# Performance work log

Hardware: AMD Instinct MI355X
Metric: run time of the kernel (lower is better)

The kernel has to match this reference:

```python
import jax, jax.numpy as jnp
from jax import lax
import numpy as np

WIN = (9, 9, 9)
NUM_CH = 5       # Ii, Ji, I2, J2, IJ stacked on channel dim, grouped conv


def setup_inputs() -> dict:
    key = jax.random.key(0)
    k1, k2 = jax.random.split(key)
    shape = (1, 1, 128, 160, 192)
    y_true = jax.random.uniform(k1, shape, dtype=jnp.float32)
    y_pred = jax.random.uniform(k2, shape, dtype=jnp.float32)
    return {"y_true": y_true, "y_pred": y_pred}


def _box_sum_3d(x, win):
    # x: [B, 5, D, H, W]
    for ax, k in enumerate(win):
        kshape = [NUM_CH, 1, 1, 1, 1]
        kshape[2 + ax] = k
        kernel = jnp.ones(kshape, x.dtype)
        pads = [(0, 0)] * 3
        pads[ax] = (k // 2, k // 2)
        x = lax.conv_general_dilated(
            x, kernel, window_strides=(1, 1, 1), padding=pads,
            dimension_numbers=("NCDHW", "OIDHW", "NCDHW"),
            feature_group_count=NUM_CH)
    return x


def reference(y_true, y_pred):
    Ii, Ji = y_true, y_pred
    stacked = jnp.concatenate([Ii, Ji, Ii * Ii, Ji * Ji, Ii * Ji], axis=1)  # [B,5,D,H,W]
    sums = _box_sum_3d(stacked, WIN)
    I_sum, J_sum, I2_sum, J2_sum, IJ_sum = jnp.split(sums, NUM_CH, axis=1)
    win_size = float(np.prod(WIN))
    cross = IJ_sum - J_sum / win_size * I_sum
    I_var = I2_sum - I_sum / win_size * I_sum
    J_var = J2_sum - J_sum / win_size * J_sum
    cc = cross * cross / (I_var * J_var + 1e-05)
    return 1.0 - jnp.mean(cc)
```

## Files before the change

kernel.cpp:

```cpp
#include <hip/hip_runtime.h>
#include <hip/hip_fp16.h>


#define D_ 128
#define H_ 160
#define W_ 192
#define WP_ (W_ / 2)
#define HW_ (H_ * W_)
#define HWP_ (HW_ / 2)
#define N_ (D_ * H_ * W_)
#define NP_ (N_ / 2)
#define WIN_INV (1.0f / 729.0f)
#define HR2 10
#define CH3 8
#define NBLK2 ((D_ * 16 * WP_) / 256)
#define NBLK3 ((HWP_ / 256) * (D_ / CH3))
#define NXCD 8

union U32H2 { unsigned u; __half2 h; };
__device__ __forceinline__ __half2 u2h(unsigned u) { U32H2 x; x.u = u; return x.h; }
__device__ __forceinline__ unsigned h2u(__half2 h) { U32H2 x; x.h = h; return x.u; }
__device__ __forceinline__ unsigned pack2(float x, float y) {
    return h2u(__float22half2_rn(make_float2(x, y)));
}
__device__ __forceinline__ float2 unpack2(unsigned u) {
    return __half22float2(u2h(u));
}

__device__ __forceinline__ void addU(float2 S[5], const uint4& q, unsigned sv) {
    float2 v0 = unpack2(q.x), v1 = unpack2(q.y), v2 = unpack2(q.z),
           v3 = unpack2(q.w), v4 = unpack2(sv);
    S[0].x += v0.x; S[0].y += v0.y;
    S[1].x += v1.x; S[1].y += v1.y;
    S[2].x += v2.x; S[2].y += v2.y;
    S[3].x += v3.x; S[3].y += v3.y;
    S[4].x += v4.x; S[4].y += v4.y;
}
__device__ __forceinline__ void subU(float2 S[5], const uint4& q, unsigned sv) {
    float2 v0 = unpack2(q.x), v1 = unpack2(q.y), v2 = unpack2(q.z),
           v3 = unpack2(q.w), v4 = unpack2(sv);
    S[0].x -= v0.x; S[0].y -= v0.y;
    S[1].x -= v1.x; S[1].y -= v1.y;
    S[2].x -= v2.x; S[2].y -= v2.y;
    S[3].x -= v3.x; S[3].y -= v3.y;
    S[4].x -= v4.x; S[4].y -= v4.y;
}

__global__ __launch_bounds__(256) void ncc_pass1(const float* __restrict__ I,
                                                 const float* __restrict__ J,
                                                 uint4* __restrict__ Aq,
                                                 unsigned* __restrict__ As,
                                                 float* __restrict__ acc) {
    __shared__ float sI[2 * W_];
    __shared__ float sJ[2 * W_];
    const int t = threadIdx.x;
    const int line0 = blockIdx.x * 2;
    const int base = line0 * W_;
    sI[t] = I[base + t];
    sJ[t] = J[base + t];
    if (t < 2 * W_ - 256) { sI[t + 256] = I[base + t + 256]; sJ[t + 256] = J[base + t + 256]; }
    if (blockIdx.x == 0 && t == 0) *acc = 0.0f;
    __syncthreads();
    if (t >= 2 * WP_) return;
    const int ll = t / WP_;
    const int wp = t % WP_;
    const int w0 = 2 * wp;
    const float* a_ = sI + ll * W_;
    const float* b_ = sJ + ll * W_;
    float s1a = 0, s2a = 0, s3a = 0, s4a = 0, s5a = 0;
    float s1b = 0, s2b = 0, s3b = 0, s4b = 0, s5b = 0;
#pragma unroll
    for (int j = -4; j <= 5; ++j) {
        int idx = w0 + j;
        float a = 0.f, b = 0.f;
        if (idx >= 0 && idx < W_) { a = a_[idx]; b = b_[idx]; }
        float p3 = a * a, p4 = b * b, p5 = a * b;
        if (j <= 4) { s1a += a; s2a += b; s3a += p3; s4a += p4; s5a += p5; }
        if (j >= -3) { s1b += a; s2b += b; s3b += p3; s4b += p4; s5b += p5; }
    }
    const size_t o = (size_t)(line0 + ll) * WP_ + wp;
    Aq[o] = make_uint4(pack2(s1a, s1b), pack2(s2a, s2b),
                       pack2(s3a, s3b), pack2(s4a, s4b));
    As[o] = pack2(s5a, s5b);
}

__global__ __launch_bounds__(256) void ncc_pass2(const uint4* __restrict__ Aq,
                                                 const unsigned* __restrict__ As,
                                                 uint4* __restrict__ Bq,
                                                 unsigned* __restrict__ Bs) {
    const int orig = (blockIdx.x % NXCD) * (NBLK2 / NXCD) + blockIdx.x / NXCD;
    const int t = orig * 256 + threadIdx.x;
    const int wp = t % WP_;
    const int r = t / WP_;
    const int hc = r & 15;
    const int d = r >> 4;
    const size_t cb = (size_t)d * (H_ * WP_) + wp;
    const uint4* aq = Aq + cb;
    const unsigned* as_ = As + cb;
    uint4* bq = Bq + cb;
    unsigned* bs = Bs + cb;
    const int h0 = hc * HR2;

    uint4 fq[9]; unsigned fs[9];
    const __half2 z = __float2half2_rn(0.f);
    __half2 S0 = z, S1 = z, S2 = z, S3 = z, S4 = z;
#pragma unroll
    for (int j = 0; j < 9; ++j) {
        int hh = h0 - 4 + j;
        uint4 q = make_uint4(0u, 0u, 0u, 0u); unsigned sv = 0u;
        if ((unsigned)hh < (unsigned)H_) {
            q = aq[(size_t)hh * WP_]; sv = as_[(size_t)hh * WP_];
        }
        fq[j] = q; fs[j] = sv;
        S0 = __hadd2(S0, u2h(q.x)); S1 = __hadd2(S1, u2h(q.y));
        S2 = __hadd2(S2, u2h(q.z)); S3 = __hadd2(S3, u2h(q.w));
        S4 = __hadd2(S4, u2h(sv));
    }
#pragma unroll
    for (int i = 0; i < HR2; ++i) {
        const int h = h0 + i;
        bq[(size_t)h * WP_] = make_uint4(h2u(S0), h2u(S1), h2u(S2), h2u(S3));
        bs[(size_t)h * WP_] = h2u(S4);
        if (i + 1 < HR2) {
            int hh = h + 5;
            uint4 q = make_uint4(0u, 0u, 0u, 0u); unsigned sv = 0u;
            if (hh < H_) { q = aq[(size_t)hh * WP_]; sv = as_[(size_t)hh * WP_]; }
            S0 = __hadd2(__hsub2(S0, u2h(fq[0].x)), u2h(q.x));
            S1 = __hadd2(__hsub2(S1, u2h(fq[0].y)), u2h(q.y));
            S2 = __hadd2(__hsub2(S2, u2h(fq[0].z)), u2h(q.z));
            S3 = __hadd2(__hsub2(S3, u2h(fq[0].w)), u2h(q.w));
            S4 = __hadd2(__hsub2(S4, u2h(fs[0])), u2h(sv));
#pragma unroll
            for (int j = 0; j < 8; ++j) { fq[j] = fq[j + 1]; fs[j] = fs[j + 1]; }
            fq[8] = q; fs[8] = sv;
        }
    }
}

__global__ __launch_bounds__(256) void ncc_pass3(const uint4* __restrict__ Bq,
                                                 const unsigned* __restrict__ Bs,
                                                 float* __restrict__ acc) {
    const int orig = (blockIdx.x % NXCD) * (NBLK3 / NXCD) + blockIdx.x / NXCD;
    const int k = orig & 7;
    const int ppBlk = orig >> 3;
    const int pp = ppBlk * 256 + threadIdx.x;
    const int d0 = k * CH3;
    const uint4* bq = Bq + pp;
    const unsigned* bs = Bs + pp;

    uint4 fq[9]; unsigned fs[9];
    float2 S[5] = {{0,0},{0,0},{0,0},{0,0},{0,0}};
#pragma unroll
    for (int j = 0; j < 9; ++j) {
        int dd = d0 - 4 + j;
        uint4 q = make_uint4(0u, 0u, 0u, 0u); unsigned sv = 0u;
        if ((unsigned)dd < (unsigned)D_) {
            q = bq[(size_t)dd * HWP_]; sv = bs[(size_t)dd * HWP_];
        }
        fq[j] = q; fs[j] = sv;
        addU(S, q, sv);
    }
    float sum = 0.f;
#pragma unroll
    for (int i = 0; i < CH3; ++i) {
        {
            float cr = S[4].x - S[1].x * S[0].x * WIN_INV;
            float Iv = S[2].x - S[0].x * S[0].x * WIN_INV;
            float Jv = S[3].x - S[1].x * S[1].x * WIN_INV;
            sum += cr * cr / (Iv * Jv + 1e-5f);
        }
        {
            float cr = S[4].y - S[1].y * S[0].y * WIN_INV;
            float Iv = S[2].y - S[0].y * S[0].y * WIN_INV;
            float Jv = S[3].y - S[1].y * S[1].y * WIN_INV;
            sum += cr * cr / (Iv * Jv + 1e-5f);
        }
        if (i + 1 < CH3) {
            int dl = d0 + i + 5;
            uint4 q = make_uint4(0u, 0u, 0u, 0u); unsigned sv = 0u;
            if (dl < D_) { q = bq[(size_t)dl * HWP_]; sv = bs[(size_t)dl * HWP_]; }
            subU(S, fq[0], fs[0]);
            addU(S, q, sv);
#pragma unroll
            for (int j = 0; j < 8; ++j) { fq[j] = fq[j + 1]; fs[j] = fs[j + 1]; }
            fq[8] = q; fs[8] = sv;
        }
    }

    for (int off = 32; off; off >>= 1) sum += __shfl_down(sum, off, 64);
    __shared__ float wsum[4];
    const int lane = threadIdx.x & 63, wv = threadIdx.x >> 6;
    if (lane == 0) wsum[wv] = sum;
    __syncthreads();
    if (threadIdx.x == 0)
        atomicAdd(acc, wsum[0] + wsum[1] + wsum[2] + wsum[3]);
}

__global__ void ncc_finalize(const float* __restrict__ acc,
                             float* __restrict__ out) {
    out[0] = 1.0f - acc[0] * (1.0f / (float)N_);
}

extern "C" void kernel_launch(void* const* d_in, const int* in_sizes, int n_in,
                              void* d_out, int out_size, void* d_ws, size_t ws_size,
                              hipStream_t stream) {
    const float* I = (const float*)d_in[0];
    const float* J = (const float*)d_in[1];
    char* w = (char*)d_ws;
    uint4* Aq = (uint4*)w;
    uint4* Bq = (uint4*)(w + (size_t)NP_ * 16);
    unsigned* As = (unsigned*)(w + (size_t)NP_ * 32);
    unsigned* Bs = (unsigned*)(w + (size_t)NP_ * 36);
    float* acc = (float*)(w + (size_t)NP_ * 40);
    float* out = (float*)d_out;

    ncc_pass1<<<D_ * H_ / 2, 256, 0, stream>>>(I, J, Aq, As, acc);
    ncc_pass2<<<NBLK2, 256, 0, stream>>>(Aq, As, Bq, Bs);
    ncc_pass3<<<NBLK3, 256, 0, stream>>>(Bq, Bs, acc);
    ncc_finalize<<<1, 1, 0, stream>>>(acc, out);
}
```

Baseline: 53.20 us.

## Fuse W and H box-sum passes via shared-memory tiles; fold finalize into pass3

```diff
diff --git a/kernel.cpp b/kernel.cpp
--- a/kernel.cpp
+++ b/kernel.cpp
@@ -11,9 +11,8 @@
 #define N_ (D_ * H_ * W_)
 #define NP_ (N_ / 2)
 #define WIN_INV (1.0f / 729.0f)
-#define HR2 10
 #define CH3 8
-#define NBLK2 ((D_ * 16 * WP_) / 256)
+#define NBLK12 (D_ * 4 * 3)
 #define NBLK3 ((HWP_ / 256) * (D_ / CH3))
 #define NXCD 8
 
@@ -46,100 +45,112 @@
     S[4].x -= v4.x; S[4].y -= v4.y;
 }
 
-__global__ __launch_bounds__(256) void ncc_pass1(const float* __restrict__ I,
-                                                 const float* __restrict__ J,
-                                                 uint4* __restrict__ Aq,
-                                                 unsigned* __restrict__ As,
-                                                 float* __restrict__ acc) {
-    __shared__ float sI[2 * W_];
-    __shared__ float sJ[2 * W_];
-    const int t = threadIdx.x;
-    const int line0 = blockIdx.x * 2;
-    const int base = line0 * W_;
-    sI[t] = I[base + t];
-    sJ[t] = J[base + t];
-    if (t < 2 * W_ - 256) { sI[t + 256] = I[base + t + 256]; sJ[t + 256] = J[base + t + 256]; }
-    if (blockIdx.x == 0 && t == 0) *acc = 0.0f;
+__global__ __launch_bounds__(256) void ncc_k12(const float* __restrict__ I,
+                                               const float* __restrict__ J,
+                                               uint4* __restrict__ Bq,
+                                               unsigned* __restrict__ Bs,
+                                               float* __restrict__ acc,
+                                               unsigned* __restrict__ ctr) {
+    __shared__ float sI[48][72];
+    __shared__ float sJ[48][72];
+    if (blockIdx.x == 0 && threadIdx.x == 0) { *acc = 0.0f; *ctr = 0u; }
+    const int orig = (blockIdx.x & 7) * (NBLK12 / NXCD) + (blockIdx.x >> 3);
+    const int d  = orig / 12;
+    const int hc = (orig / 3) & 3;
+    const int wc = orig % 3;
+    const int h0 = hc * 40;
+    const int wbase = wc * 64;
+    const float* Ib = I + (size_t)d * HW_;
+    const float* Jb = J + (size_t)d * HW_;
+
+    for (int i = threadIdx.x; i < 48 * 36; i += 256) {
+        const int r = i / 36, c2 = i % 36;
+        const int h = h0 - 4 + r;
+        const int w = wbase - 4 + 2 * c2;
+        float2 vi = make_float2(0.f, 0.f), vj = make_float2(0.f, 0.f);
+        if ((unsigned)h < (unsigned)H_ && (unsigned)w < (unsigned)(W_ - 1)) {
+            vi = *(const float2*)(Ib + h * W_ + w);
+            vj = *(const float2*)(Jb + h * W_ + w);
+        }
+        sI[r][2 * c2] = vi.x; sI[r][2 * c2 + 1] = vi.y;
+        sJ[r][2 * c2] = vj.x; sJ[r][2 * c2 + 1] = vj.y;
+    }
     __syncthreads();
-    if (t >= 2 * WP_) return;
-    const int ll = t / WP_;
-    const int wp = t % WP_;
-    const int w0 = 2 * wp;
-    const float* a_ = sI + ll * W_;
-    const float* b_ = sJ + ll * W_;
-    float s1a = 0, s2a = 0, s3a = 0, s4a = 0, s5a = 0;
-    float s1b = 0, s2b = 0, s3b = 0, s4b = 0, s5b = 0;
-#pragma unroll
-    for (int j = -4; j <= 5; ++j) {
-        int idx = w0 + j;
-        float a = 0.f, b = 0.f;
-        if (idx >= 0 && idx < W_) { a = a_[idx]; b = b_[idx]; }
-        float p3 = a * a, p4 = b * b, p5 = a * b;
-        if (j <= 4) { s1a += a; s2a += b; s3a += p3; s4a += p4; s5a += p5; }
-        if (j >= -3) { s1b += a; s2b += b; s3b += p3; s4b += p4; s5b += p5; }
-    }
-    const size_t o = (size_t)(line0 + ll) * WP_ + wp;
-    Aq[o] = make_uint4(pack2(s1a, s1b), pack2(s2a, s2b),
-                       pack2(s3a, s3b), pack2(s4a, s4b));
-    As[o] = pack2(s5a, s5b);
-}
-
-__global__ __launch_bounds__(256) void ncc_pass2(const uint4* __restrict__ Aq,
-                                                 const unsigned* __restrict__ As,
-                                                 uint4* __restrict__ Bq,
-                                                 unsigned* __restrict__ Bs) {
-    const int orig = (blockIdx.x % NXCD) * (NBLK2 / NXCD) + blockIdx.x / NXCD;
-    const int t = orig * 256 + threadIdx.x;
-    const int wp = t % WP_;
-    const int r = t / WP_;
-    const int hc = r & 15;
-    const int d = r >> 4;
-    const size_t cb = (size_t)d * (H_ * WP_) + wp;
-    const uint4* aq = Aq + cb;
-    const unsigned* as_ = As + cb;
-    uint4* bq = Bq + cb;
-    unsigned* bs = Bs + cb;
-    const int h0 = hc * HR2;
-
-    uint4 fq[9]; unsigned fs[9];
+
+    const int wp = threadIdx.x & 31;
+    const int hslot = threadIdx.x >> 5;
+    const int rb = hslot * 5;
+
+    auto rowsum = [&](int r, uint4& q, unsigned& sv) {
+        const float* ri = &sI[r][2 * wp];
+        const float* rj = &sJ[r][2 * wp];
+        float a[10], b[10];
+#pragma unroll
+        for (int k = 0; k < 5; ++k) {
+            float2 va = *(const float2*)(ri + 2 * k);
+            float2 vb = *(const float2*)(rj + 2 * k);
+            a[2 * k] = va.x; a[2 * k + 1] = va.y;
+            b[2 * k] = vb.x; b[2 * k + 1] = vb.y;
+        }
+        float s1 = 0, s2 = 0, s3 = 0, s4 = 0, s5 = 0;
+#pragma unroll
+        for (int k = 0; k < 9; ++k) {
+            s1 += a[k]; s2 += b[k];
+            s3 += a[k] * a[k]; s4 += b[k] * b[k]; s5 += a[k] * b[k];
+        }
+        const float t1 = s1 - a[0] + a[9];
+        const float t2 = s2 - b[0] + b[9];
+        const float t3 = s3 - a[0] * a[0] + a[9] * a[9];
+        const float t4 = s4 - b[0] * b[0] + b[9] * b[9];
+        const float t5 = s5 - a[0] * b[0] + a[9] * b[9];
+        q = make_uint4(pack2(s1, t1), pack2(s2, t2), pack2(s3, t3), pack2(s4, t4));
+        sv = pack2(s5, t5);
+    };
+
+    uint4 w0q, w1q, w2q, w3q; unsigned w0s, w1s, w2s, w3s;
     const __half2 z = __float2half2_rn(0.f);
     __half2 S0 = z, S1 = z, S2 = z, S3 = z, S4 = z;
-#pragma unroll
-    for (int j = 0; j < 9; ++j) {
-        int hh = h0 - 4 + j;
-        uint4 q = make_uint4(0u, 0u, 0u, 0u); unsigned sv = 0u;
-        if ((unsigned)hh < (unsigned)H_) {
-            q = aq[(size_t)hh * WP_]; sv = as_[(size_t)hh * WP_];
-        }
-        fq[j] = q; fs[j] = sv;
-        S0 = __hadd2(S0, u2h(q.x)); S1 = __hadd2(S1, u2h(q.y));
-        S2 = __hadd2(S2, u2h(q.z)); S3 = __hadd2(S3, u2h(q.w));
-        S4 = __hadd2(S4, u2h(sv));
-    }
-#pragma unroll
-    for (int i = 0; i < HR2; ++i) {
-        const int h = h0 + i;
-        bq[(size_t)h * WP_] = make_uint4(h2u(S0), h2u(S1), h2u(S2), h2u(S3));
-        bs[(size_t)h * WP_] = h2u(S4);
-        if (i + 1 < HR2) {
-            int hh = h + 5;
-            uint4 q = make_uint4(0u, 0u, 0u, 0u); unsigned sv = 0u;
-            if (hh < H_) { q = aq[(size_t)hh * WP_]; sv = as_[(size_t)hh * WP_]; }
-            S0 = __hadd2(__hsub2(S0, u2h(fq[0].x)), u2h(q.x));
-            S1 = __hadd2(__hsub2(S1, u2h(fq[0].y)), u2h(q.y));
-            S2 = __hadd2(__hsub2(S2, u2h(fq[0].z)), u2h(q.z));
-            S3 = __hadd2(__hsub2(S3, u2h(fq[0].w)), u2h(q.w));
-            S4 = __hadd2(__hsub2(S4, u2h(fs[0])), u2h(sv));
-#pragma unroll
-            for (int j = 0; j < 8; ++j) { fq[j] = fq[j + 1]; fs[j] = fs[j + 1]; }
-            fq[8] = q; fs[8] = sv;
+    {
+        uint4 q; unsigned sv;
+#pragma unroll
+        for (int j = 0; j < 9; ++j) {
+            rowsum(rb + j, q, sv);
+            if (j == 0) { w0q = q; w0s = sv; }
+            if (j == 1) { w1q = q; w1s = sv; }
+            if (j == 2) { w2q = q; w2s = sv; }
+            if (j == 3) { w3q = q; w3s = sv; }
+            S0 = __hadd2(S0, u2h(q.x)); S1 = __hadd2(S1, u2h(q.y));
+            S2 = __hadd2(S2, u2h(q.z)); S3 = __hadd2(S3, u2h(q.w));
+            S4 = __hadd2(S4, u2h(sv));
+        }
+    }
+
+    const int wpg = wc * 32 + wp;
+    const size_t ob0 = (size_t)d * (H_ * WP_) + (size_t)(h0 + rb) * WP_ + wpg;
+#pragma unroll
+    for (int i = 0; i < 5; ++i) {
+        const size_t o = ob0 + (size_t)i * WP_;
+        Bq[o] = make_uint4(h2u(S0), h2u(S1), h2u(S2), h2u(S3));
+        Bs[o] = h2u(S4);
+        if (i < 4) {
+            uint4 q; unsigned sv;
+            rowsum(rb + 9 + i, q, sv);
+            const uint4  oq = (i == 0) ? w0q : (i == 1) ? w1q : (i == 2) ? w2q : w3q;
+            const unsigned os = (i == 0) ? w0s : (i == 1) ? w1s : (i == 2) ? w2s : w3s;
+            S0 = __hadd2(__hsub2(S0, u2h(oq.x)), u2h(q.x));
+            S1 = __hadd2(__hsub2(S1, u2h(oq.y)), u2h(q.y));
+            S2 = __hadd2(__hsub2(S2, u2h(oq.z)), u2h(q.z));
+            S3 = __hadd2(__hsub2(S3, u2h(oq.w)), u2h(q.w));
+            S4 = __hadd2(__hsub2(S4, u2h(os)),   u2h(sv));
         }
     }
 }
 
 __global__ __launch_bounds__(256) void ncc_pass3(const uint4* __restrict__ Bq,
                                                  const unsigned* __restrict__ Bs,
-                                                 float* __restrict__ acc) {
+                                                 float* __restrict__ acc,
+                                                 unsigned* __restrict__ ctr,
+                                                 float* __restrict__ out) {
     const int orig = (blockIdx.x % NXCD) * (NBLK3 / NXCD) + blockIdx.x / NXCD;
     const int k = orig & 7;
     const int ppBlk = orig >> 3;
@@ -192,13 +203,15 @@
     const int lane = threadIdx.x & 63, wv = threadIdx.x >> 6;
     if (lane == 0) wsum[wv] = sum;
     __syncthreads();
-    if (threadIdx.x == 0)
-        atomicAdd(acc, wsum[0] + wsum[1] + wsum[2] + wsum[3]);
-}
-
-__global__ void ncc_finalize(const float* __restrict__ acc,
-                             float* __restrict__ out) {
-    out[0] = 1.0f - acc[0] * (1.0f / (float)N_);
+    if (threadIdx.x == 0) {
+        float old = atomicAdd(acc, wsum[0] + wsum[1] + wsum[2] + wsum[3]);
+        asm volatile("" :: "v"(old));
+        unsigned t = atomicAdd(ctr, 1u);
+        if (t == NBLK3 - 1) {
+            float tot = atomicAdd(acc, 0.0f);
+            out[0] = 1.0f - tot * (1.0f / (float)N_);
+        }
+    }
 }
 
 extern "C" void kernel_launch(void* const* d_in, const int* in_sizes, int n_in,
@@ -207,15 +220,12 @@
     const float* I = (const float*)d_in[0];
     const float* J = (const float*)d_in[1];
     char* w = (char*)d_ws;
-    uint4* Aq = (uint4*)w;
-    uint4* Bq = (uint4*)(w + (size_t)NP_ * 16);
-    unsigned* As = (unsigned*)(w + (size_t)NP_ * 32);
-    unsigned* Bs = (unsigned*)(w + (size_t)NP_ * 36);
-    float* acc = (float*)(w + (size_t)NP_ * 40);
+    uint4* Bq = (uint4*)w;
+    unsigned* Bs = (unsigned*)(w + (size_t)NP_ * 16);
+    float* acc = (float*)(w + (size_t)NP_ * 20);
+    unsigned* ctr = (unsigned*)(w + (size_t)NP_ * 20 + 4);
     float* out = (float*)d_out;
 
-    ncc_pass1<<<D_ * H_ / 2, 256, 0, stream>>>(I, J, Aq, As, acc);
-    ncc_pass2<<<NBLK2, 256, 0, stream>>>(Aq, As, Bq, Bs);
-    ncc_pass3<<<NBLK3, 256, 0, stream>>>(Bq, Bs, acc);
-    ncc_finalize<<<1, 1, 0, stream>>>(acc, out);
-}
+    ncc_k12<<<NBLK12, 256, 0, stream>>>(I, J, Bq, Bs, acc, ctr);
+    ncc_pass3<<<NBLK3, 256, 0, stream>>>(Bq, Bs, acc, ctr, out);
+}
```

After: 56.48 us. 6.2% more time.
